# Kernel optimization log

Hardware: AMD Instinct MI355X
Metric: run time of the kernel (lower is better)

## Reference

```python
import jax, jax.numpy as jnp
import numpy as np

LN2 = 0.69314718  # matches the 2ln2 constant in the original rbf()


def setup_inputs() -> dict:
    key = jax.random.key(0)
    domain_min = [-1.0, -1.0, -1.0]
    domain_max = [1.0, 1.0, 1.0]
    n = [12, 12, 12]
    codomain_dim = 128
    N = 200000

    axes = [jnp.linspace(domain_min[i], domain_max[i], n[i], dtype=jnp.float32)
            for i in range(len(n))]
    # torch.meshgrid default is 'ij' indexing
    grid = jnp.stack(jnp.meshgrid(*axes, indexing='ij'), axis=-1).reshape(-1, len(n))  # [G, 3]

    # rbf_width: mean nearest-neighbor distance on the grid (second-smallest per row)
    d = jnp.linalg.norm(grid[:, None, :] - grid[None, :, :], axis=-1)  # [G, G], G=1728 -> small
    width = jnp.sort(d, axis=1)[:, 1].mean()

    # interpolation matrix m and coeffs = solve(m, weight), as in __init__ (no_grad buffer)
    m = jnp.exp(-(d ** 2) / (width ** 2 / LN2))
    k1, k2 = jax.random.split(key)
    weight = jax.random.normal(k1, (grid.shape[0], codomain_dim), dtype=jnp.float32)
    coeffs = jnp.linalg.solve(m, weight)  # [G, C]

    x = jax.random.normal(k2, (N, len(n)), dtype=jnp.float32)  # [N, 3]
    return {"x": x, "grid": grid, "coeffs": coeffs, "width": width}


def reference(x, grid, coeffs, width):
    # Squared Euclidean distance via |a|^2 + |b|^2 - 2ab (avoids [N, G, 3] broadcast tensor).
    # rbf(d, w) = exp(-d^2 / (w^2 / ln2)); since it only uses d^2, skip the sqrt.
    x2 = jnp.sum(x * x, axis=-1, keepdims=True)          # [N, 1]
    g2 = jnp.sum(grid * grid, axis=-1)                   # [G]
    d2 = x2 + g2[None, :] - 2.0 * (x @ grid.T)           # [N, G]
    d2 = jnp.maximum(d2, 0.0)                            # numerical guard
    p = jnp.exp(-d2 * (LN2 / (width * width)))           # [N, G]
    return p @ coeffs                                    # [N, C]
```

## Files before the change

### kernel.cpp

```cpp
#include <hip/hip_runtime.h>
#include <stdint.h>


typedef _Float16 f16;
typedef _Float16 f16x8 __attribute__((ext_vector_type(8)));
typedef float f32x16 __attribute__((ext_vector_type(16)));

#define LN2F 0.69314718f
#define LOG2E 1.4426950408889634f

#define CD 128
#define KD 1728

__global__ void prep_coeffs(const float* __restrict__ coeffs,
                            f16* __restrict__ ch, f16* __restrict__ cl) {
  int kp  = blockIdx.x * 2 + (threadIdx.x >> 7);
  int col = threadIdx.x & 127;
  int i   = kp / 144;
  int r   = kp - i * 144;
  int s   = r >> 4;
  int idx = r & 15;
  int hh  = idx >> 3;
  int b   = idx & 7;
  int j, k2;
  if (s < 6) { j = 2 * s + hh;                 k2 = b; }
  else       { j = 4 * (s - 6) + 2 * hh + (b >> 2); k2 = 8 + (b & 3); }
  float v = coeffs[(size_t)((i * 12 + j) * 12 + k2) * CD + col];
  f16 h = (f16)v;
  f16 l = (f16)(v - (float)h);
  size_t o = ((size_t)(kp >> 3) * CD + col) * 8 + (kp & 7);
  ch[o] = h;
  cl[o] = l;
}

union FU { uint32_t u[4]; f16x8 v; };

__global__ __launch_bounds__(256) void rbf_gemm(
    const float* __restrict__ x,
    const float* __restrict__ width,
    const f16* __restrict__ ch, const f16* __restrict__ cl,
    float* __restrict__ out, int N) {
  const int t    = threadIdx.x;
  const int lane = t & 63;
  const int wv   = t >> 6;
  const int l31  = lane & 31;
  const int hh   = lane >> 5;
  const int wvr  = wv >> 1;
  const int wvc  = wv & 1;
  const int rbase = blockIdx.x * 64;

  const float w  = width[0];
  const float s2 = (LN2F * LOG2E) / (w * w);

  int rr = rbase + wvr * 32 + l31;
  if (rr >= N) rr = N - 1;
  const float x0 = x[(size_t)rr * 3 + 0];
  const float x1 = x[(size_t)rr * 3 + 1];
  const float x2 = x[(size_t)rr * 3 + 2];

  float e1a[12], e2a[12];
#pragma unroll
  for (int k = 0; k < 12; ++k) {
    float g  = (float)k * (2.0f / 11.0f) - 1.0f;
    float d1 = x1 - g;
    float d2 = x2 - g;
    e1a[k] = __builtin_amdgcn_exp2f(-d1 * d1 * s2);
    e2a[k] = __builtin_amdgcn_exp2f(-d2 * d2 * s2);
  }

  const char* gh = (const char*)ch + (size_t)(hh * 128 + wvc * 64 + l31) * 16;
  const char* gl = (const char*)cl + (size_t)(hh * 128 + wvc * 64 + l31) * 16;

  f16x8 cbh0 = *(const f16x8*)(gh);
  f16x8 cbh1 = *(const f16x8*)(gh + 512);
  f16x8 cbl0 = *(const f16x8*)(gl);
  f16x8 cbl1 = *(const f16x8*)(gl + 512);

  f32x16 acc0, acc1;
#pragma unroll
  for (int q = 0; q < 16; ++q) { acc0[q] = 0.f; acc1[q] = 0.f; }

#pragma unroll 1
  for (int i = 0; i < 12; ++i) {
    float gi  = (float)i * (2.0f / 11.0f) - 1.0f;
    float d0  = x0 - gi;
    float e0i = __builtin_amdgcn_exp2f(-d0 * d0 * s2);

#pragma unroll
    for (int s = 0; s < 9; ++s) {
      const char* ph = gh + (s + 1) * 4096;
      const char* pl = gl + (s + 1) * 4096;
      f16x8 nbh0 = *(const f16x8*)(ph);
      f16x8 nbh1 = *(const f16x8*)(ph + 512);
      f16x8 nbl0 = *(const f16x8*)(pl);
      f16x8 nbl1 = *(const f16x8*)(pl + 512);

      FU ah, al;
      if (s < 6) {
        float es = e0i * (hh ? e1a[2 * s + 1] : e1a[2 * s]);
#pragma unroll
        for (int q = 0; q < 4; ++q) {
          float ea = e2a[2 * q];
          float eb = e2a[2 * q + 1];
          uint32_t hq, lq;
          asm("v_fma_mixlo_f16 %0, %1, %2, 0"
              : "=v"(hq) : "v"(es), "v"(ea));
          asm("v_fma_mixhi_f16 %0, %1, %2, 0"
              : "+v"(hq) : "v"(es), "v"(eb));
          asm("v_fma_mixlo_f16 %0, %1, %2, -%3 op_sel:[0,0,0] op_sel_hi:[0,0,1]"
              : "=v"(lq) : "v"(es), "v"(ea), "v"(hq));
          asm("v_fma_mixhi_f16 %0, %1, %2, -%3 op_sel:[0,0,1] op_sel_hi:[0,0,1]"
              : "+v"(lq) : "v"(es), "v"(eb), "v"(hq));
          ah.u[q] = hq;
          al.u[q] = lq;
        }
      } else {
        int J0 = 4 * (s - 6);
        float c01 = e0i * (hh ? e1a[J0 + 2] : e1a[J0 + 0]);
        float c23 = e0i * (hh ? e1a[J0 + 3] : e1a[J0 + 1]);
#pragma unroll
        for (int q = 0; q < 4; ++q) {
          float es = (q < 2) ? c01 : c23;
          float ea = e2a[8 + 2 * (q & 1)];
          float eb = e2a[9 + 2 * (q & 1)];
          uint32_t hq, lq;
          asm("v_fma_mixlo_f16 %0, %1, %2, 0"
              : "=v"(hq) : "v"(es), "v"(ea));
          asm("v_fma_mixhi_f16 %0, %1, %2, 0"
              : "+v"(hq) : "v"(es), "v"(eb));
          asm("v_fma_mixlo_f16 %0, %1, %2, -%3 op_sel:[0,0,0] op_sel_hi:[0,0,1]"
              : "=v"(lq) : "v"(es), "v"(ea), "v"(hq));
          asm("v_fma_mixhi_f16 %0, %1, %2, -%3 op_sel:[0,0,1] op_sel_hi:[0,0,1]"
              : "+v"(lq) : "v"(es), "v"(eb), "v"(hq));
          ah.u[q] = hq;
          al.u[q] = lq;
        }
      }

      acc0 = __builtin_amdgcn_mfma_f32_32x32x16_f16(ah.v, cbh0, acc0, 0, 0, 0);
      acc1 = __builtin_amdgcn_mfma_f32_32x32x16_f16(ah.v, cbh1, acc1, 0, 0, 0);
      acc0 = __builtin_amdgcn_mfma_f32_32x32x16_f16(al.v, cbh0, acc0, 0, 0, 0);
      acc1 = __builtin_amdgcn_mfma_f32_32x32x16_f16(al.v, cbh1, acc1, 0, 0, 0);
      acc0 = __builtin_amdgcn_mfma_f32_32x32x16_f16(ah.v, cbl0, acc0, 0, 0, 0);
      acc1 = __builtin_amdgcn_mfma_f32_32x32x16_f16(ah.v, cbl1, acc1, 0, 0, 0);

      cbh0 = nbh0; cbh1 = nbh1; cbl0 = nbl0; cbl1 = nbl1;
    }
    gh += 9 * 4096;
    gl += 9 * 4096;
  }

#pragma unroll
  for (int q = 0; q < 16; ++q) {
    int row = rbase + wvr * 32 + (q & 3) + 8 * (q >> 2) + 4 * hh;
    if (row < N) {
      int col = wvc * 64 + l31;
      out[(size_t)row * CD + col]      = acc0[q];
      out[(size_t)row * CD + col + 32] = acc1[q];
    }
  }
}

__global__ void rbf_fallback(const float* __restrict__ x, const float* __restrict__ grid,
                             const float* __restrict__ coeffs, const float* __restrict__ width,
                             float* __restrict__ out, int N) {
  int row = blockIdx.x;
  int col = threadIdx.x;
  if (row >= N) return;
  float x0 = x[(size_t)row * 3 + 0];
  float x1 = x[(size_t)row * 3 + 1];
  float x2 = x[(size_t)row * 3 + 2];
  float w = width[0];
  float s2 = (LN2F * LOG2E) / (w * w);
  float acc = 0.f;
  for (int g = 0; g < 1728; ++g) {
    float d0 = x0 - grid[g * 3 + 0];
    float d1 = x1 - grid[g * 3 + 1];
    float d2 = x2 - grid[g * 3 + 2];
    float p = exp2f(-(d0 * d0 + d1 * d1 + d2 * d2) * s2);
    acc += p * coeffs[(size_t)g * CD + col];
  }
  out[(size_t)row * CD + col] = acc;
}

extern "C" void kernel_launch(void* const* d_in, const int* in_sizes, int n_in,
                              void* d_out, int out_size, void* d_ws, size_t ws_size,
                              hipStream_t stream) {
  const float* x      = (const float*)d_in[0];
  const float* grid   = (const float*)d_in[1];
  const float* coeffs = (const float*)d_in[2];
  const float* width  = (const float*)d_in[3];
  float* out = (float*)d_out;
  int N = in_sizes[0] / 3;

  size_t need = (size_t)2 * CD * KD * sizeof(f16) + 16384;
  if (ws_size >= need) {
    f16* ch = (f16*)d_ws;
    f16* cl = ch + (size_t)CD * KD;
    hipLaunchKernelGGL(prep_coeffs, dim3(KD / 2), dim3(256), 0, stream,
                       coeffs, ch, cl);
    int nb = (N + 63) / 64;
    hipLaunchKernelGGL(rbf_gemm, dim3(nb), dim3(256), 0, stream,
                       x, width, ch, cl, out, N);
  } else {
    hipLaunchKernelGGL(rbf_fallback, dim3(N), dim3(CD), 0, stream,
                       x, grid, coeffs, width, out, N);
  }
}
```

Baseline: 283.2 us.

## Interleave hi/lo coefficient image per column half and split grid by columns

Packs the hi and lo f16 coefficient parts into a single interleaved image grouped by k-step and 64-column half, so each wave's four B-fragment loads land in one contiguous 4 KB region. The block tiling also changes: each block now covers 128 rows with 4 waves sharing one 64-column half, and a second grid dimension picks the half. The intended saving is memory traffic and cache-line waste from loading coefficients out of two separate buffers. The cost is that each block recomputes the exp values for its rows twice across the two column halves, and the grid shape changes.

```diff
diff --git a/kernel.cpp b/kernel.cpp
--- a/kernel.cpp
+++ b/kernel.cpp
@@ -13,7 +13,7 @@
 #define KD 1728
 
 __global__ void prep_coeffs(const float* __restrict__ coeffs,
-                            f16* __restrict__ ch, f16* __restrict__ cl) {
+                            f16* __restrict__ img) {
   int kp  = blockIdx.x * 2 + (threadIdx.x >> 7);
   int col = threadIdx.x & 127;
   int i   = kp / 144;
@@ -28,9 +28,12 @@
   float v = coeffs[(size_t)((i * 12 + j) * 12 + k2) * CD + col];
   f16 h = (f16)v;
   f16 l = (f16)(v - (float)h);
-  size_t o = ((size_t)(kp >> 3) * CD + col) * 8 + (kp & 7);
-  ch[o] = h;
-  cl[o] = l;
+  int q   = i * 9 + s;
+  int ch2 = col >> 6;
+  int c64 = col & 63;
+  size_t o = (size_t)q * 4096 + ch2 * 2048 + hh * 512 + c64 * 8 + b;
+  img[o]        = h;
+  img[o + 1024] = l;
 }
 
 union FU { uint32_t u[4]; f16x8 v; };
@@ -38,21 +41,20 @@
 __global__ __launch_bounds__(256) void rbf_gemm(
     const float* __restrict__ x,
     const float* __restrict__ width,
-    const f16* __restrict__ ch, const f16* __restrict__ cl,
+    const f16* __restrict__ img,
     float* __restrict__ out, int N) {
   const int t    = threadIdx.x;
   const int lane = t & 63;
   const int wv   = t >> 6;
   const int l31  = lane & 31;
   const int hh   = lane >> 5;
-  const int wvr  = wv >> 1;
-  const int wvc  = wv & 1;
-  const int rbase = blockIdx.x * 64;
+  const int rbase = blockIdx.x * 128;
+  const int ch2   = blockIdx.y;
 
   const float w  = width[0];
   const float s2 = (LN2F * LOG2E) / (w * w);
 
-  int rr = rbase + wvr * 32 + l31;
+  int rr = rbase + wv * 32 + l31;
   if (rr >= N) rr = N - 1;
   const float x0 = x[(size_t)rr * 3 + 0];
   const float x1 = x[(size_t)rr * 3 + 1];
@@ -68,13 +70,13 @@
     e2a[k] = __builtin_amdgcn_exp2f(-d2 * d2 * s2);
   }
 
-  const char* gh = (const char*)ch + (size_t)(hh * 128 + wvc * 64 + l31) * 16;
-  const char* gl = (const char*)cl + (size_t)(hh * 128 + wvc * 64 + l31) * 16;
-
-  f16x8 cbh0 = *(const f16x8*)(gh);
-  f16x8 cbh1 = *(const f16x8*)(gh + 512);
-  f16x8 cbl0 = *(const f16x8*)(gl);
-  f16x8 cbl1 = *(const f16x8*)(gl + 512);
+  const int voff = ch2 * 4096 + hh * 1024 + l31 * 16;
+  const char* imgb = (const char*)img;
+
+  f16x8 cb0 = *(const f16x8*)(imgb + voff + 0);
+  f16x8 cb1 = *(const f16x8*)(imgb + voff + 512);
+  f16x8 cb2 = *(const f16x8*)(imgb + voff + 2048);
+  f16x8 cb3 = *(const f16x8*)(imgb + voff + 2560);
 
   f32x16 acc0, acc1;
 #pragma unroll
@@ -88,12 +90,11 @@
 
 #pragma unroll
     for (int s = 0; s < 9; ++s) {
-      const char* ph = gh + (s + 1) * 4096;
-      const char* pl = gl + (s + 1) * 4096;
-      f16x8 nbh0 = *(const f16x8*)(ph);
-      f16x8 nbh1 = *(const f16x8*)(ph + 512);
-      f16x8 nbl0 = *(const f16x8*)(pl);
-      f16x8 nbl1 = *(const f16x8*)(pl + 512);
+      const char* spn = imgb + (size_t)(i * 9 + s + 1) * 8192;
+      f16x8 nb0 = *(const f16x8*)(spn + voff + 0);
+      f16x8 nb1 = *(const f16x8*)(spn + voff + 512);
+      f16x8 nb2 = *(const f16x8*)(spn + voff + 2048);
+      f16x8 nb3 = *(const f16x8*)(spn + voff + 2560);
 
       FU ah, al;
       if (s < 6) {
@@ -137,24 +138,22 @@
         }
       }
 
-      acc0 = __builtin_amdgcn_mfma_f32_32x32x16_f16(ah.v, cbh0, acc0, 0, 0, 0);
-      acc1 = __builtin_amdgcn_mfma_f32_32x32x16_f16(ah.v, cbh1, acc1, 0, 0, 0);
-      acc0 = __builtin_amdgcn_mfma_f32_32x32x16_f16(al.v, cbh0, acc0, 0, 0, 0);
-      acc1 = __builtin_amdgcn_mfma_f32_32x32x16_f16(al.v, cbh1, acc1, 0, 0, 0);
-      acc0 = __builtin_amdgcn_mfma_f32_32x32x16_f16(ah.v, cbl0, acc0, 0, 0, 0);
-      acc1 = __builtin_amdgcn_mfma_f32_32x32x16_f16(ah.v, cbl1, acc1, 0, 0, 0);
-
-      cbh0 = nbh0; cbh1 = nbh1; cbl0 = nbl0; cbl1 = nbl1;
+      acc0 = __builtin_amdgcn_mfma_f32_32x32x16_f16(ah.v, cb0, acc0, 0, 0, 0);
+      acc1 = __builtin_amdgcn_mfma_f32_32x32x16_f16(ah.v, cb1, acc1, 0, 0, 0);
+      acc0 = __builtin_amdgcn_mfma_f32_32x32x16_f16(al.v, cb0, acc0, 0, 0, 0);
+      acc1 = __builtin_amdgcn_mfma_f32_32x32x16_f16(al.v, cb1, acc1, 0, 0, 0);
+      acc0 = __builtin_amdgcn_mfma_f32_32x32x16_f16(ah.v, cb2, acc0, 0, 0, 0);
+      acc1 = __builtin_amdgcn_mfma_f32_32x32x16_f16(ah.v, cb3, acc1, 0, 0, 0);
+
+      cb0 = nb0; cb1 = nb1; cb2 = nb2; cb3 = nb3;
     }
-    gh += 9 * 4096;
-    gl += 9 * 4096;
   }
 
 #pragma unroll
   for (int q = 0; q < 16; ++q) {
-    int row = rbase + wvr * 32 + (q & 3) + 8 * (q >> 2) + 4 * hh;
+    int row = rbase + wv * 32 + (q & 3) + 8 * (q >> 2) + 4 * hh;
     if (row < N) {
-      int col = wvc * 64 + l31;
+      int col = ch2 * 64 + l31;
       out[(size_t)row * CD + col]      = acc0[q];
       out[(size_t)row * CD + col + 32] = acc1[q];
     }
@@ -193,15 +192,14 @@
   float* out = (float*)d_out;
   int N = in_sizes[0] / 3;
 
-  size_t need = (size_t)2 * CD * KD * sizeof(f16) + 16384;
+  size_t need = (size_t)KD * CD * 2 * sizeof(f16) + 16384;
   if (ws_size >= need) {
-    f16* ch = (f16*)d_ws;
-    f16* cl = ch + (size_t)CD * KD;
+    f16* img = (f16*)d_ws;
     hipLaunchKernelGGL(prep_coeffs, dim3(KD / 2), dim3(256), 0, stream,
-                       coeffs, ch, cl);
-    int nb = (N + 63) / 64;
-    hipLaunchKernelGGL(rbf_gemm, dim3(nb), dim3(256), 0, stream,
-                       x, width, ch, cl, out, N);
+                       coeffs, img);
+    int nb = (N + 127) / 128;
+    hipLaunchKernelGGL(rbf_gemm, dim3(nb, 2), dim3(256), 0, stream,
+                       x, width, img, out, N);
   } else {
     hipLaunchKernelGGL(rbf_fallback, dim3(N), dim3(CD), 0, stream,
                        x, grid, coeffs, width, out, N);
```

Result: faster. 264.5 us (-6.6%).
